# Kernel optimization log

Hardware: AMD Instinct MI355X
Metric: run time of the kernel (lower is better)

The kernel has to match this reference:

```python
import jax, jax.numpy as jnp
import numpy as np


def _malvar_kernels():
    g_at_rb = np.array([[0,0,-1,0,0],[0,0,2,0,0],[-1,2,4,2,-1],[0,0,2,0,0],[0,0,-1,0,0]], np.float32) / 8.0
    rb_at_g_col = np.array([[0,0,0.5,0,0],[0,-1,0,-1,0],[-1,4,5,4,-1],[0,-1,0,-1,0],[0,0,0.5,0,0]], np.float32) / 8.0
    rb_at_g_row = np.array([[0,0,-1,0,0],[0,-1,4,-1,0],[0.5,0,5,0,0.5],[0,-1,4,-1,0],[0,0,-1,0,0]], np.float32) / 8.0
    rb_at_br = np.array([[0,0,-1.5,0,0],[0,2,0,2,0],[-1.5,0,6,0,-1.5],[0,2,0,2,0],[0,0,-1.5,0,0]], np.float32) / 8.0
    r = lambda k: jnp.asarray(k).reshape(1, 1, 5, 5)  # OIHW
    return r(g_at_rb), r(rb_at_g_col), r(rb_at_g_row), r(rb_at_br)


def setup_inputs() -> dict:
    key = jax.random.key(0)
    B, H, W = 8, 2048, 2048
    bayer = jax.random.uniform(key, (B, 1, H, W), dtype=jnp.float32)
    kg, kcol, krow, kbr = _malvar_kernels()
    return {"bayer": bayer, "k_g_at_rb": kg, "k_rb_at_g_col": kcol,
            "k_rb_at_g_row": krow, "k_rb_at_br": kbr}


def _conv(x, k):
    return jax.lax.conv_general_dilated(
        x, k, window_strides=(1, 1), padding='VALID',
        dimension_numbers=('NCHW', 'OIHW', 'NCHW'))


def _masks(H, W, dtype):
    # RGGB parity masks, shape [1,1,H,W]
    ii = (jnp.arange(H) % 2)[:, None]
    jj = (jnp.arange(W) % 2)[None, :]
    f = lambda m: m.astype(dtype)[None, None]
    r_mask = f((ii == 0) & (jj == 0))
    gr_mask = f((ii == 0) & (jj == 1))
    gb_mask = f((ii == 1) & (jj == 0))
    b_mask = f((ii == 1) & (jj == 1))
    return r_mask, gr_mask, gb_mask, b_mask


def reference(bayer, k_g_at_rb, k_rb_at_g_col, k_rb_at_g_row, k_rb_at_br):
    B, C, H, W = bayer.shape
    pad = jnp.pad(bayer, ((0, 0), (0, 0), (2, 2), (2, 2)), mode='reflect')
    r_mask, gr_mask, gb_mask, b_mask = _masks(H, W, bayer.dtype)
    g_mask = gr_mask + gb_mask
    # 4 distinct 5x5 convs (torch version launches 7 but 3 are duplicates)
    g_at_rb = _conv(pad, k_g_at_rb.astype(bayer.dtype))
    at_g_col = _conv(pad, k_rb_at_g_col.astype(bayer.dtype))  # r@Gr, b@Gb
    at_g_row = _conv(pad, k_rb_at_g_row.astype(bayer.dtype))  # r@Gb, b@Gr
    at_br = _conv(pad, k_rb_at_br.astype(bayer.dtype))        # r@B, b@R
    red = bayer * r_mask + at_g_col * gr_mask + at_g_row * gb_mask + at_br * b_mask
    green = bayer * g_mask + g_at_rb * r_mask + g_at_rb * b_mask
    blue = bayer * b_mask + at_g_row * gr_mask + at_g_col * gb_mask + at_br * r_mask
    rgb = jnp.concatenate([red, green, blue], axis=1)
    return jnp.clip(rgb, 0.0, 1.0)
```

## Files before the change

### kernel.cpp

```cpp
#include <hip/hip_runtime.h>


typedef float f4 __attribute__((ext_vector_type(4)));

__device__ __forceinline__ int reflect_idx(int i, int n) {
    if (i < 0) i = -i;
    if (i >= n) i = 2 * n - 2 - i;
    return i;
}

__device__ __forceinline__ float clip01(float x) {
    return fminf(fmaxf(x, 0.0f), 1.0f);
}

struct Halo { float m2, m1, p4, p5; };

__device__ __forceinline__ Halo make_halo(f4 x, f4 xl, f4 xr,
                                          bool lane0, bool lane63,
                                          bool ledge, bool redge) {
    Halo h;
    h.m2 = __shfl_up(x.z, 1);
    h.m1 = __shfl_up(x.w, 1);
    if (lane0) { h.m2 = xl.z; h.m1 = xl.w; }
    if (ledge) { h.m2 = x.z;  h.m1 = x.y; }
    h.p4 = __shfl_down(x.x, 1);
    h.p5 = __shfl_down(x.y, 1);
    if (lane63) { h.p4 = xr.x; h.p5 = xr.y; }
    if (redge)  { h.p4 = x.z;  h.p5 = x.y; }
    return h;
}

template <bool EVEN_ROW>
__device__ __forceinline__ void compute4(
    const float C[8], const float S13[8], const float S04[8],
    float r[4], float g[4], float b[4]) {
#pragma unroll
    for (int k = 0; k < 4; k += 2) {
        const int c = 2 + k, o = 3 + k;
        const int ce = EVEN_ROW ? c : o;
        const int co = EVEN_ROW ? o : c;
        const float t2 = S04[ce] + C[ce - 2] + C[ce + 2];
        const float gatrb = 0.5f * C[ce]
                          + 0.25f * (S13[ce] + C[ce - 1] + C[ce + 1])
                          - 0.125f * t2;
        const float brv   = 0.75f * C[ce]
                          + 0.25f * (S13[ce - 1] + S13[ce + 1])
                          - 0.1875f * t2;
        const float t4 = C[co - 1] + C[co + 1];
        const float t5 = S13[co - 1] + S13[co + 1];
        const float t6 = C[co - 2] + C[co + 2];
        const float colv = 0.625f * C[co] + 0.5f * t4
                         - 0.125f * (t5 + t6) + 0.0625f * S04[co];
        const float rowv = 0.625f * C[co] + 0.5f * S13[co]
                         - 0.125f * t5 - 0.125f * S04[co] + 0.0625f * t6;
        if (EVEN_ROW) {
            r[k] = C[c];      g[k] = gatrb;      b[k] = brv;
            r[k + 1] = colv;  g[k + 1] = C[o];   b[k + 1] = rowv;
        } else {
            r[k] = rowv;      g[k] = C[c];       b[k] = colv;
            r[k + 1] = brv;   g[k + 1] = gatrb;  b[k + 1] = C[o];
        }
    }
}

__global__ __launch_bounds__(256, 6) void demosaic_kernel(
    const float* __restrict__ bayer, float* __restrict__ out, int H, int W) {
    const int bid = blockIdx.x;
    const int chunk = gridDim.x >> 3;
    const int lin = (bid & 7) * chunk + (bid >> 3);
    const int XT = W >> 10;
    const int xt = lin % XT;
    const int rowlin = lin / XT;
    const int y = rowlin % H;
    const int img = rowlin / H;

    const int tid = (int)threadIdx.x;
    const int lane = tid & 63;
    const bool lane0 = (lane == 0), lane63 = (lane == 63);
    const int x0 = xt * 1024 + (tid << 2);
    const bool ledge = (x0 == 0);
    const bool redge = (x0 + 4 == W);

    const size_t plane = (size_t)H * W;
    const float* src = bayer + (size_t)img * plane;

    const float* rows[5];
#pragma unroll
    for (int i = 0; i < 5; ++i)
        rows[i] = src + (size_t)reflect_idx(y - 2 + i, H) * W;

    f4 a0 = *(const f4*)(rows[0] + x0);
    f4 a1 = *(const f4*)(rows[1] + x0);
    f4 a2 = *(const f4*)(rows[2] + x0);
    f4 a3 = *(const f4*)(rows[3] + x0);
    f4 a4 = *(const f4*)(rows[4] + x0);

    f4 LC = {0,0,0,0}, LS13 = {0,0,0,0}, LS04 = {0,0,0,0};
    f4 RC = {0,0,0,0}, RS13 = {0,0,0,0}, RS04 = {0,0,0,0};
    if (lane0 && !ledge) {
        f4 l0 = *(const f4*)(rows[0] + x0 - 4);
        f4 l1 = *(const f4*)(rows[1] + x0 - 4);
        f4 l2 = *(const f4*)(rows[2] + x0 - 4);
        f4 l3 = *(const f4*)(rows[3] + x0 - 4);
        f4 l4 = *(const f4*)(rows[4] + x0 - 4);
        LC = l2; LS13 = l1 + l3; LS04 = l0 + l4;
    }
    if (lane63 && !redge) {
        f4 r0 = *(const f4*)(rows[0] + x0 + 4);
        f4 r1 = *(const f4*)(rows[1] + x0 + 4);
        f4 r2 = *(const f4*)(rows[2] + x0 + 4);
        f4 r3 = *(const f4*)(rows[3] + x0 + 4);
        f4 r4 = *(const f4*)(rows[4] + x0 + 4);
        RC = r2; RS13 = r1 + r3; RS04 = r0 + r4;
    }

    const f4 Cc  = a2;
    const f4 S13 = a1 + a3;
    const f4 S04 = a0 + a4;

    const Halo hC  = make_halo(Cc,  LC,  RC,  lane0, lane63, ledge, redge);
    const Halo h13 = make_halo(S13, LS13, RS13, lane0, lane63, ledge, redge);
    const Halo h04 = make_halo(S04, LS04, RS04, lane0, lane63, ledge, redge);

    const float Cw[8]  = {hC.m2,  hC.m1,  Cc.x,  Cc.y,  Cc.z,  Cc.w,  hC.p4,  hC.p5};
    const float W13[8] = {h13.m2, h13.m1, S13.x, S13.y, S13.z, S13.w, h13.p4, h13.p5};
    const float W04[8] = {h04.m2, h04.m1, S04.x, S04.y, S04.z, S04.w, h04.p4, h04.p5};

    float r[4], g[4], b[4];
    if ((y & 1) == 0) compute4<true>(Cw, W13, W04, r, g, b);
    else              compute4<false>(Cw, W13, W04, r, g, b);

    float* o = out + (size_t)img * 3 * plane + (size_t)y * W + x0;
    f4 vr = {clip01(r[0]), clip01(r[1]), clip01(r[2]), clip01(r[3])};
    f4 vg = {clip01(g[0]), clip01(g[1]), clip01(g[2]), clip01(g[3])};
    f4 vb = {clip01(b[0]), clip01(b[1]), clip01(b[2]), clip01(b[3])};
    __builtin_nontemporal_store(vr, (f4*)(o));
    __builtin_nontemporal_store(vg, (f4*)(o + plane));
    __builtin_nontemporal_store(vb, (f4*)(o + 2 * plane));
}

extern "C" void kernel_launch(void* const* d_in, const int* in_sizes, int n_in,
                              void* d_out, int out_size, void* d_ws, size_t ws_size,
                              hipStream_t stream) {
    const float* bayer = (const float*)d_in[0];
    float* out = (float*)d_out;

    const int H = 2048, W = 2048;
    const int B = in_sizes[0] / (H * W);
    const int XT = W >> 10;

    dim3 block(256, 1, 1);
    dim3 grid(B * H * XT, 1, 1);
    demosaic_kernel<<<grid, block, 0, stream>>>(bayer, out, H, W);
}
```

Baseline: 75.85 us.

## Process two output rows per thread to reuse vertically overlapping input rows

Each thread now computes an even and an odd output row together, loading six input rows instead of five per row. Four of those rows are shared between the two rows, which cuts redundant global and L2 loads and removes the runtime parity branch. The grid is halved and launch bounds drop from 6 to 4 waves, so there is less parallelism per launch and more register pressure per thread.

```diff
diff --git a/kernel.cpp b/kernel.cpp
--- a/kernel.cpp
+++ b/kernel.cpp
@@ -63,7 +63,32 @@
     }
 }
 
-__global__ __launch_bounds__(256, 6) void demosaic_kernel(
+template <bool EVEN_ROW>
+__device__ __forceinline__ void do_row(
+    f4 Cc, f4 S13, f4 S04,
+    f4 LC, f4 LS13, f4 LS04, f4 RC, f4 RS13, f4 RS04,
+    bool lane0, bool lane63, bool ledge, bool redge,
+    float* __restrict__ o, size_t plane) {
+    const Halo hC  = make_halo(Cc,  LC,  RC,  lane0, lane63, ledge, redge);
+    const Halo h13 = make_halo(S13, LS13, RS13, lane0, lane63, ledge, redge);
+    const Halo h04 = make_halo(S04, LS04, RS04, lane0, lane63, ledge, redge);
+
+    const float Cw[8]  = {hC.m2,  hC.m1,  Cc.x,  Cc.y,  Cc.z,  Cc.w,  hC.p4,  hC.p5};
+    const float W13[8] = {h13.m2, h13.m1, S13.x, S13.y, S13.z, S13.w, h13.p4, h13.p5};
+    const float W04[8] = {h04.m2, h04.m1, S04.x, S04.y, S04.z, S04.w, h04.p4, h04.p5};
+
+    float r[4], g[4], b[4];
+    compute4<EVEN_ROW>(Cw, W13, W04, r, g, b);
+
+    f4 vr = {clip01(r[0]), clip01(r[1]), clip01(r[2]), clip01(r[3])};
+    f4 vg = {clip01(g[0]), clip01(g[1]), clip01(g[2]), clip01(g[3])};
+    f4 vb = {clip01(b[0]), clip01(b[1]), clip01(b[2]), clip01(b[3])};
+    __builtin_nontemporal_store(vr, (f4*)(o));
+    __builtin_nontemporal_store(vg, (f4*)(o + plane));
+    __builtin_nontemporal_store(vb, (f4*)(o + 2 * plane));
+}
+
+__global__ __launch_bounds__(256, 4) void demosaic_kernel(
     const float* __restrict__ bayer, float* __restrict__ out, int H, int W) {
     const int bid = blockIdx.x;
     const int chunk = gridDim.x >> 3;
@@ -71,8 +96,9 @@
     const int XT = W >> 10;
     const int xt = lin % XT;
     const int rowlin = lin / XT;
-    const int y = rowlin % H;
-    const int img = rowlin / H;
+    const int Hp = H >> 1;
+    const int y0 = (rowlin % Hp) << 1;
+    const int img = rowlin / Hp;
 
     const int tid = (int)threadIdx.x;
     const int lane = tid & 63;
@@ -84,26 +110,31 @@
     const size_t plane = (size_t)H * W;
     const float* src = bayer + (size_t)img * plane;
 
-    const float* rows[5];
+    const float* rows[6];
 #pragma unroll
-    for (int i = 0; i < 5; ++i)
-        rows[i] = src + (size_t)reflect_idx(y - 2 + i, H) * W;
+    for (int i = 0; i < 6; ++i)
+        rows[i] = src + (size_t)reflect_idx(y0 - 2 + i, H) * W;
 
     f4 a0 = *(const f4*)(rows[0] + x0);
     f4 a1 = *(const f4*)(rows[1] + x0);
     f4 a2 = *(const f4*)(rows[2] + x0);
     f4 a3 = *(const f4*)(rows[3] + x0);
     f4 a4 = *(const f4*)(rows[4] + x0);
+    f4 a5 = *(const f4*)(rows[5] + x0);
 
-    f4 LC = {0,0,0,0}, LS13 = {0,0,0,0}, LS04 = {0,0,0,0};
-    f4 RC = {0,0,0,0}, RS13 = {0,0,0,0}, RS04 = {0,0,0,0};
+    f4 LCe = {0,0,0,0}, LS13e = {0,0,0,0}, LS04e = {0,0,0,0};
+    f4 LCo = {0,0,0,0}, LS13o = {0,0,0,0}, LS04o = {0,0,0,0};
+    f4 RCe = {0,0,0,0}, RS13e = {0,0,0,0}, RS04e = {0,0,0,0};
+    f4 RCo = {0,0,0,0}, RS13o = {0,0,0,0}, RS04o = {0,0,0,0};
     if (lane0 && !ledge) {
         f4 l0 = *(const f4*)(rows[0] + x0 - 4);
         f4 l1 = *(const f4*)(rows[1] + x0 - 4);
         f4 l2 = *(const f4*)(rows[2] + x0 - 4);
         f4 l3 = *(const f4*)(rows[3] + x0 - 4);
         f4 l4 = *(const f4*)(rows[4] + x0 - 4);
-        LC = l2; LS13 = l1 + l3; LS04 = l0 + l4;
+        f4 l5 = *(const f4*)(rows[5] + x0 - 4);
+        LCe = l2; LS13e = l1 + l3; LS04e = l0 + l4;
+        LCo = l3; LS13o = l2 + l4; LS04o = l1 + l5;
     }
     if (lane63 && !redge) {
         f4 r0 = *(const f4*)(rows[0] + x0 + 4);
@@ -111,32 +142,19 @@
         f4 r2 = *(const f4*)(rows[2] + x0 + 4);
         f4 r3 = *(const f4*)(rows[3] + x0 + 4);
         f4 r4 = *(const f4*)(rows[4] + x0 + 4);
-        RC = r2; RS13 = r1 + r3; RS04 = r0 + r4;
+        f4 r5 = *(const f4*)(rows[5] + x0 + 4);
+        RCe = r2; RS13e = r1 + r3; RS04e = r0 + r4;
+        RCo = r3; RS13o = r2 + r4; RS04o = r1 + r5;
     }
 
-    const f4 Cc  = a2;
-    const f4 S13 = a1 + a3;
-    const f4 S04 = a0 + a4;
+    float* o = out + (size_t)img * 3 * plane + (size_t)y0 * W + x0;
 
-    const Halo hC  = make_halo(Cc,  LC,  RC,  lane0, lane63, ledge, redge);
-    const Halo h13 = make_halo(S13, LS13, RS13, lane0, lane63, ledge, redge);
-    const Halo h04 = make_halo(S04, LS04, RS04, lane0, lane63, ledge, redge);
-
-    const float Cw[8]  = {hC.m2,  hC.m1,  Cc.x,  Cc.y,  Cc.z,  Cc.w,  hC.p4,  hC.p5};
-    const float W13[8] = {h13.m2, h13.m1, S13.x, S13.y, S13.z, S13.w, h13.p4, h13.p5};
-    const float W04[8] = {h04.m2, h04.m1, S04.x, S04.y, S04.z, S04.w, h04.p4, h04.p5};
-
-    float r[4], g[4], b[4];
-    if ((y & 1) == 0) compute4<true>(Cw, W13, W04, r, g, b);
-    else              compute4<false>(Cw, W13, W04, r, g, b);
-
-    float* o = out + (size_t)img * 3 * plane + (size_t)y * W + x0;
-    f4 vr = {clip01(r[0]), clip01(r[1]), clip01(r[2]), clip01(r[3])};
-    f4 vg = {clip01(g[0]), clip01(g[1]), clip01(g[2]), clip01(g[3])};
-    f4 vb = {clip01(b[0]), clip01(b[1]), clip01(b[2]), clip01(b[3])};
-    __builtin_nontemporal_store(vr, (f4*)(o));
-    __builtin_nontemporal_store(vg, (f4*)(o + plane));
-    __builtin_nontemporal_store(vb, (f4*)(o + 2 * plane));
+    do_row<true>(a2, a1 + a3, a0 + a4,
+                 LCe, LS13e, LS04e, RCe, RS13e, RS04e,
+                 lane0, lane63, ledge, redge, o, plane);
+    do_row<false>(a3, a2 + a4, a1 + a5,
+                  LCo, LS13o, LS04o, RCo, RS13o, RS04o,
+                  lane0, lane63, ledge, redge, o + W, plane);
 }
 
 extern "C" void kernel_launch(void* const* d_in, const int* in_sizes, int n_in,
@@ -150,6 +168,6 @@
     const int XT = W >> 10;
 
     dim3 block(256, 1, 1);
-    dim3 grid(B * H * XT, 1, 1);
+    dim3 grid(B * (H >> 1) * XT, 1, 1);
     demosaic_kernel<<<grid, block, 0, stream>>>(bayer, out, H, W);
 }
```

After: 79.99 us. 1.05x slower.
